# Optimization experiments

Hardware: AMD Instinct MI355X
Metric: run time of the kernel (lower is better)

Reference implementation:

```python
import jax, jax.numpy as jnp
import numpy as np

B, CI, CO, H, W, M1, M2 = 4, 64, 64, 256, 256, 16, 16


def setup_inputs() -> dict:
    key = jax.random.key(0)
    k0, k1, k2, k3, k4 = jax.random.split(key, 5)
    scale = 1.0 / (CI * CO)
    x = jax.random.normal(k0, (B, CI, H, W), dtype=jnp.float32)
    # torch.rand -> uniform [0,1), scaled; real/imag parts of complex weights
    w1r = scale * jax.random.uniform(k1, (CO, CI, M1, M2), dtype=jnp.float32)
    w1i = scale * jax.random.uniform(k2, (CO, CI, M1, M2), dtype=jnp.float32)
    w2r = scale * jax.random.uniform(k3, (CO, CI, M1, M2), dtype=jnp.float32)
    w2i = scale * jax.random.uniform(k4, (CO, CI, M1, M2), dtype=jnp.float32)
    return {"x": x, "w1r": w1r, "w1i": w1i, "w2r": w2r, "w2i": w2i}


def reference(x, w1r, w1i, w2r, w2i):
    b, ci, h, w = x.shape
    co, _, m1, m2 = w1r.shape
    wf = w // 2 + 1  # rfft width
    x_ft = jnp.fft.rfft2(x)                       # [b, ci, h, wf] complex
    xs = x_ft[:, :, :m1, :m2]                     # low-frequency slice
    w1 = w1r + 1j * w1i
    w2 = w2r + 1j * w2i
    o1 = jnp.einsum('bixy,ioxy->boxy', xs, w1)    # [b, co, m1, m2]
    o2 = jnp.einsum('bixy,ioxy->boxy', xs, w2)    # same slice, per original code
    out_ft = jnp.zeros((b, co, h, wf), dtype=x_ft.dtype)
    out_ft = out_ft.at[:, :, :m1, :m2].set(o1)
    out_ft = out_ft.at[:, :, h - m1:, :m2].set(o2)
    return jnp.fft.irfft2(out_ft, s=(h, w))
```

## Files before the change

### kernel.cpp

```cpp
#include <hip/hip_runtime.h>

#define NB 4
#define NCI 64
#define NCO 64
#define PLANE 65536

#define OF_XS_RE 0
#define OF_XS_IM (OF_XS_RE + PLANE)
#define OF_O1_RE (OF_XS_IM + PLANE)
#define OF_O1_IM (OF_O1_RE + PLANE)
#define OF_O2_RE (OF_O1_IM + PLANE)
#define OF_O2_IM (OF_O2_RE + PLANE)

#define XEOFF(w) ((w)*260)
#define XOOFF(w) (16*260 + 8 + (w)*260)

#define TPF 6.2831853071795864769f

__global__ __launch_bounds__(1024, 4) void k12_dft(const float* __restrict__ x,
                                                   float* __restrict__ ws) {
  __shared__ float bufA[8336], bufB[8336];
  __shared__ float cst[256], snt[256];
  __shared__ float2 s2[1024];
  const int t = threadIdx.x;
  const int img = blockIdx.x;

  if (t < 256) {
    float sv_, cv_;
    sincosf(TPF * (float)t * (1.0f/256.0f), &sv_, &cv_);
    cst[t] = cv_;  snt[t] = sv_;
  }

  const int sl = t & 3, row = t >> 2;
  const int wq = t & 3, p = (t >> 2) & 1;
  const int kg = (t >> 3) & 1, tr = t >> 4;
  int kyv[4];
#pragma unroll
  for (int j = 0; j < 4; ++j) kyv[j] = p + 8*kg + 2*j;

  const float* xb = x + (size_t)img * 65536;

  float4 lo0 = *(const float4*)(xb + row*256 + sl*4);
  float4 hi0 = *(const float4*)(xb + row*256 + 128 + sl*4);
  float4 lo1 = *(const float4*)(xb + row*256 + 16 + sl*4);
  float4 hi1 = *(const float4*)(xb + row*256 + 144 + sl*4);

  __syncthreads();

  float cd[4], sd[4];
#pragma unroll
  for (int j = 0; j < 4; ++j) { cd[j] = cst[kyv[j]]; sd[j] = snt[kyv[j]]; }

  float ar[4][4], ai[4][4];
#pragma unroll
  for (int j = 0; j < 4; ++j)
#pragma unroll
    for (int r = 0; r < 4; ++r) { ar[j][r] = 0.f; ai[j][r] = 0.f; }

  bufA[XEOFF(sl*4+0) + row] = lo0.x + hi0.x;
  bufA[XEOFF(sl*4+1) + row] = lo0.y + hi0.y;
  bufA[XEOFF(sl*4+2) + row] = lo0.z + hi0.z;
  bufA[XEOFF(sl*4+3) + row] = lo0.w + hi0.w;
  bufA[XOOFF(sl*4+0) + row] = lo0.x - hi0.x;
  bufA[XOOFF(sl*4+1) + row] = lo0.y - hi0.y;
  bufA[XOOFF(sl*4+2) + row] = lo0.z - hi0.z;
  bufA[XOOFF(sl*4+3) + row] = lo0.w - hi0.w;
  __syncthreads();

  const int pofs = p ? (16*260 + 8) : 0;

  for (int c = 0; c < 8; ++c) {
    float* cur = (c & 1) ? bufB : bufA;
    float* nxt = (c & 1) ? bufA : bufB;
    if (c < 6) {
      const int w0n = (c+2) * 16;
      if (c & 1) {
        lo1 = *(const float4*)(xb + row*256 + w0n + sl*4);
        hi1 = *(const float4*)(xb + row*256 + w0n + 128 + sl*4);
      } else {
        lo0 = *(const float4*)(xb + row*256 + w0n + sl*4);
        hi0 = *(const float4*)(xb + row*256 + w0n + 128 + sl*4);
      }
    }
    float cc[4], sv[4];
#pragma unroll
    for (int j = 0; j < 4; ++j) {
      const int m = (kyv[j] * (c*16 + wq*4)) & 255;
      cc[j] = cst[m];
      sv[j] = snt[m];
    }
    const float* rp = cur + pofs;
#pragma unroll
    for (int i = 0; i < 4; ++i) {
      const int wl = wq*4 + i;
      const float4 xs4 = *(const float4*)&rp[wl*260 + tr*4];
#pragma unroll
      for (int j = 0; j < 4; ++j) {
        ar[j][0] += xs4.x * cc[j];  ai[j][0] -= xs4.x * sv[j];
        ar[j][1] += xs4.y * cc[j];  ai[j][1] -= xs4.y * sv[j];
        ar[j][2] += xs4.z * cc[j];  ai[j][2] -= xs4.z * sv[j];
        ar[j][3] += xs4.w * cc[j];  ai[j][3] -= xs4.w * sv[j];
        const float nc = cc[j]*cd[j] - sv[j]*sd[j];
        const float ns = sv[j]*cd[j] + cc[j]*sd[j];
        cc[j] = nc; sv[j] = ns;
      }
    }
    if (c < 7) {
      if (c & 1) {
        nxt[XEOFF(sl*4+0) + row] = lo0.x + hi0.x;
        nxt[XEOFF(sl*4+1) + row] = lo0.y + hi0.y;
        nxt[XEOFF(sl*4+2) + row] = lo0.z + hi0.z;
        nxt[XEOFF(sl*4+3) + row] = lo0.w + hi0.w;
        nxt[XOOFF(sl*4+0) + row] = lo0.x - hi0.x;
        nxt[XOOFF(sl*4+1) + row] = lo0.y - hi0.y;
        nxt[XOOFF(sl*4+2) + row] = lo0.z - hi0.z;
        nxt[XOOFF(sl*4+3) + row] = lo0.w - hi0.w;
      } else {
        nxt[XEOFF(sl*4+0) + row] = lo1.x + hi1.x;
        nxt[XEOFF(sl*4+1) + row] = lo1.y + hi1.y;
        nxt[XEOFF(sl*4+2) + row] = lo1.z + hi1.z;
        nxt[XEOFF(sl*4+3) + row] = lo1.w + hi1.w;
        nxt[XOOFF(sl*4+0) + row] = lo1.x - hi1.x;
        nxt[XOOFF(sl*4+1) + row] = lo1.y - hi1.y;
        nxt[XOOFF(sl*4+2) + row] = lo1.z - hi1.z;
        nxt[XOOFF(sl*4+3) + row] = lo1.w - hi1.w;
      }
    }
    __syncthreads();
  }

#pragma unroll
  for (int j = 0; j < 4; ++j)
#pragma unroll
    for (int r = 0; r < 4; ++r) {
      ar[j][r] += __shfl_xor(ar[j][r], 1);
      ar[j][r] += __shfl_xor(ar[j][r], 2);
      ai[j][r] += __shfl_xor(ai[j][r], 1);
      ai[j][r] += __shfl_xor(ai[j][r], 2);
    }
  if (wq == 0) {
#pragma unroll
    for (int j = 0; j < 4; ++j) {
      const int ky = kyv[j];
      float4 sr; sr.x = ar[j][0]; sr.y = ar[j][1]; sr.z = ar[j][2]; sr.w = ar[j][3];
      float4 si; si.x = ai[j][0]; si.y = ai[j][1]; si.z = ai[j][2]; si.w = ai[j][3];
      *(float4*)&bufA[XEOFF(ky) + tr*4] = sr;
      *(float4*)&bufA[XOOFF(ky) + tr*4] = si;
    }
  }
  __syncthreads();

  const int ky2 = t & 15, kx = (t >> 4) & 15, hh = t >> 8;
  const float sg = (kx & 1) ? -1.f : 1.f;
  const float cdk = cst[kx], sdk = snt[kx];
  const int m0 = (kx * hh * 32) & 255;
  float cR = cst[m0], sR = snt[m0];
  float arr = 0.f, aii = 0.f;
  const int be = XEOFF(ky2) + hh*32;
  const int bo = XOOFF(ky2) + hh*32;
#pragma unroll 4
  for (int hq = 0; hq < 8; ++hq) {
    const float4 xrL = *(const float4*)&bufA[be + hq*4];
    const float4 xrH = *(const float4*)&bufA[be + 128 + hq*4];
    const float4 xiL = *(const float4*)&bufA[bo + hq*4];
    const float4 xiH = *(const float4*)&bufA[bo + 128 + hq*4];
    {
      const float xr = xrL.x + sg*xrH.x, xi = xiL.x + sg*xiH.x;
      arr += xr*cR + xi*sR;  aii += xi*cR - xr*sR;
      const float nc = cR*cdk - sR*sdk, ns = sR*cdk + cR*sdk; cR = nc; sR = ns;
    }
    {
      const float xr = xrL.y + sg*xrH.y, xi = xiL.y + sg*xiH.y;
      arr += xr*cR + xi*sR;  aii += xi*cR - xr*sR;
      const float nc = cR*cdk - sR*sdk, ns = sR*cdk + cR*sdk; cR = nc; sR = ns;
    }
    {
      const float xr = xrL.z + sg*xrH.z, xi = xiL.z + sg*xiH.z;
      arr += xr*cR + xi*sR;  aii += xi*cR - xr*sR;
      const float nc = cR*cdk - sR*sdk, ns = sR*cdk + cR*sdk; cR = nc; sR = ns;
    }
    {
      const float xr = xrL.w + sg*xrH.w, xi = xiL.w + sg*xiH.w;
      arr += xr*cR + xi*sR;  aii += xi*cR - xr*sR;
      const float nc = cR*cdk - sR*sdk, ns = sR*cdk + cR*sdk; cR = nc; sR = ns;
    }
  }
  s2[t].x = arr; s2[t].y = aii;
  __syncthreads();
  if (t < 256) {
    float xre = s2[t].x + s2[t+256].x + s2[t+512].x + s2[t+768].x;
    float xim = s2[t].y + s2[t+256].y + s2[t+512].y + s2[t+768].y;
    ws[OF_XS_RE + img*256 + t] = xre;
    ws[OF_XS_IM + img*256 + t] = xim;
  }
}

__global__ __launch_bounds__(256) void k3_mix(const float* __restrict__ w1r,
    const float* __restrict__ w1i, const float* __restrict__ w2r,
    const float* __restrict__ w2i, float* __restrict__ ws) {
  const int o  = blockIdx.x;
  const int mc = blockIdx.y;
  const int t  = threadIdx.x;
  const int b  = t >> 6;
  const int m  = (mc << 6) + (t & 63);
  const float* xsr = ws + OF_XS_RE;
  const float* xsi = ws + OF_XS_IM;
  float a1r=0.f, a1i=0.f, a2r=0.f, a2i=0.f;
#pragma unroll 4
  for (int i = 0; i < NCI; ++i) {
    const float xr = xsr[((b*NCI + i) << 8) + m];
    const float xi = xsi[((b*NCI + i) << 8) + m];
    const int wi = ((i*NCO + o) << 8) + m;
    const float p = w1r[wi], q = w1i[wi], u = w2r[wi], v = w2i[wi];
    a1r += xr*p - xi*q;
    a1i += xr*q + xi*p;
    a2r += xr*u - xi*v;
    a2i += xr*v + xi*u;
  }
  const int oi = ((b*NCO + o) << 8) + m;
  ws[OF_O1_RE + oi] = a1r;
  ws[OF_O1_IM + oi] = a1i;
  ws[OF_O2_RE + oi] = a2r;
  ws[OF_O2_IM + oi] = a2i;
}

__global__ __launch_bounds__(256) void k45_idft(const float* __restrict__ ws,
                                                float* __restrict__ out) {
  __shared__ __align__(16) float o1r[256], o1i[256], o2r[256], o2i[256];
  __shared__ float cst[256], snt[256];
  __shared__ __align__(16) float Sr[128][20], Si[128][20];
  const int t   = threadIdx.x;
  const int bo  = blockIdx.x >> 1;
  const int hcc = blockIdx.x & 1;

  o1r[t] = ws[OF_O1_RE + bo*256 + t];
  o1i[t] = ws[OF_O1_IM + bo*256 + t];
  o2r[t] = ws[OF_O2_RE + bo*256 + t];
  o2i[t] = ws[OF_O2_IM + bo*256 + t];
  {
    float sv_, cv_;
    sincosf(TPF * (float)t * (1.0f/256.0f), &sv_, &cv_);
    cst[t] = cv_;  snt[t] = sv_;
  }
  __syncthreads();

  {
    const int hl = t >> 2, kq = t & 3;
    const int h  = hcc*64 + hl;
    const float chh = cst[h], shh = snt[h];
    float c1 = 1.f, s1 = 0.f;
    const int m2i = (240 * h) & 255;
    float cB = cst[m2i], sB = snt[m2i];
    float4 srE = {0,0,0,0}, siE = {0,0,0,0};
    float4 srO = {0,0,0,0}, siO = {0,0,0,0};
#pragma unroll
    for (int j = 0; j < 16; ++j) {
      const float4 r1 = *(const float4*)&o1r[j*16 + kq*4];
      const float4 i1 = *(const float4*)&o1i[j*16 + kq*4];
      const float4 r2 = *(const float4*)&o2r[j*16 + kq*4];
      const float4 i2 = *(const float4*)&o2i[j*16 + kq*4];
      float4& sr = (j & 1) ? srO : srE;
      float4& si = (j & 1) ? siO : siE;
      sr.x += r1.x*c1 - i1.x*s1 + r2.x*cB - i2.x*sB;
      si.x += r1.x*s1 + i1.x*c1 + r2.x*sB + i2.x*cB;
      sr.y += r1.y*c1 - i1.y*s1 + r2.y*cB - i2.y*sB;
      si.y += r1.y*s1 + i1.y*c1 + r2.y*sB + i2.y*cB;
      sr.z += r1.z*c1 - i1.z*s1 + r2.z*cB - i2.z*sB;
      si.z += r1.z*s1 + i1.z*c1 + r2.z*sB + i2.z*cB;
      sr.w += r1.w*c1 - i1.w*s1 + r2.w*cB - i2.w*sB;
      si.w += r1.w*s1 + i1.w*c1 + r2.w*sB + i2.w*cB;
      const float n1c = c1*chh - s1*shh, n1s = s1*chh + c1*shh;
      const float n2c = cB*chh - sB*shh, n2s = sB*chh + cB*shh;
      c1 = n1c; s1 = n1s; cB = n2c; sB = n2s;
    }
    float4 sp, sm;
    sp.x = srE.x + srO.x; sp.y = srE.y + srO.y; sp.z = srE.z + srO.z; sp.w = srE.w + srO.w;
    sm.x = srE.x - srO.x; sm.y = srE.y - srO.y; sm.z = srE.z - srO.z; sm.w = srE.w - srO.w;
    *(float4*)&Sr[hl][kq*4]      = sp;
    *(float4*)&Sr[hl+64][kq*4]   = sm;
    sp.x = siE.x + siO.x; sp.y = siE.y + siO.y; sp.z = siE.z + siO.z; sp.w = siE.w + siO.w;
    sm.x = siE.x - siO.x; sm.y = siE.y - siO.y; sm.z = siE.z - siO.z; sm.w = siE.w - siO.w;
    *(float4*)&Si[hl][kq*4]      = sp;
    *(float4*)&Si[hl+64][kq*4]   = sm;
  }
  __syncthreads();

  const int wl = t & 31;
  float c[15], s[15], c2[15], s2[15];
#pragma unroll
  for (int k = 0; k < 15; ++k) {
    const int mi = ((k+1) * wl) & 255;
    c[k] = cst[mi];
    s[k] = snt[mi];
  }
  {
    const float R = 0.70710678118654752f;
#pragma unroll
    for (int k = 0; k < 15; ++k) {
      const int r8 = (k + 1) & 7;
      switch (r8) {
        case 0: c2[k] =  c[k];            s2[k] =  s[k];            break;
        case 1: c2[k] = (c[k]-s[k])*R;    s2[k] = (s[k]+c[k])*R;    break;
        case 2: c2[k] = -s[k];            s2[k] =  c[k];            break;
        case 3: c2[k] = -(c[k]+s[k])*R;   s2[k] = (c[k]-s[k])*R;    break;
        case 4: c2[k] = -c[k];            s2[k] = -s[k];            break;
        case 5: c2[k] = (s[k]-c[k])*R;    s2[k] = -(c[k]+s[k])*R;   break;
        case 6: c2[k] =  s[k];            s2[k] = -c[k];            break;
        default:c2[k] = (c[k]+s[k])*R;    s2[k] = (s[k]-c[k])*R;    break;
      }
    }
  }

  const int half = (t >> 5) & 1;
  const int wv = t >> 6;
  const float scale = 2.0f / 65536.0f;
  const size_t base256 = (size_t)bo*256 + hcc*64;
#pragma unroll 2
  for (int pr = 0; pr < 16; ++pr) {
    const int lr = wv*32 + pr*2 + half;
    const float4 a0 = *(const float4*)&Sr[lr][0];
    const float4 a1 = *(const float4*)&Sr[lr][4];
    const float4 a2 = *(const float4*)&Sr[lr][8];
    const float4 a3 = *(const float4*)&Sr[lr][12];
    const float4 b0 = *(const float4*)&Si[lr][0];
    const float4 b1 = *(const float4*)&Si[lr][4];
    const float4 b2 = *(const float4*)&Si[lr][8];
    const float4 b3 = *(const float4*)&Si[lr][12];
    const float re[16] = {a0.x,a0.y,a0.z,a0.w, a1.x,a1.y,a1.z,a1.w,
                          a2.x,a2.y,a2.z,a2.w, a3.x,a3.y,a3.z,a3.w};
    const float im[16] = {b0.x,b0.y,b0.z,b0.w, b1.x,b1.y,b1.z,b1.w,
                          b2.x,b2.y,b2.z,b2.w, b3.x,b3.y,b3.z,b3.w};
    const int grow = (lr & 63) + ((lr >> 6) << 7);
    const size_t ob = (base256 + grow) * 256;

#pragma unroll
    for (int g = 0; g < 2; ++g) {
      const float* cc = g ? c2 : c;
      const float* ss = g ? s2 : s;
      float PA = 0.5f * re[0];
      float PB = 0.f, PC = 0.f, PD = 0.f, QB = 0.f, QD = 0.f;
#pragma unroll
      for (int k = 0; k < 15; ++k) {
        const int ky = k + 1;
        const float R = re[ky], I = im[ky];
        const int cls = ky & 3;
        if (cls == 0)      PA += R*cc[k] - I*ss[k];
        else if (cls == 1) { PB += R*cc[k] - I*ss[k];  QB += R*ss[k] + I*cc[k]; }
        else if (cls == 2) PC += R*cc[k] - I*ss[k];
        else               { PD += R*cc[k] - I*ss[k];  QD += R*ss[k] + I*cc[k]; }
      }
      const float T1 = PA + PC, T2 = PB + PD;
      const float T3 = PA - PC, T4 = QB - QD;
      const int cb = wl + g*32;
      out[ob + cb]       = (T1 + T2) * scale;
      out[ob + cb + 64]  = (T3 - T4) * scale;
      out[ob + cb + 128] = (T1 - T2) * scale;
      out[ob + cb + 192] = (T3 + T4) * scale;
    }
  }
}

extern "C" void kernel_launch(void* const* d_in, const int* in_sizes, int n_in,
                              void* d_out, int out_size, void* d_ws, size_t ws_size,
                              hipStream_t stream) {
  const float* x   = (const float*)d_in[0];
  const float* w1r = (const float*)d_in[1];
  const float* w1i = (const float*)d_in[2];
  const float* w2r = (const float*)d_in[3];
  const float* w2i = (const float*)d_in[4];
  float* out = (float*)d_out;
  float* ws  = (float*)d_ws;

  hipLaunchKernelGGL(k12_dft,  dim3(256),   dim3(1024), 0, stream, x, ws);
  hipLaunchKernelGGL(k3_mix,   dim3(64, 4), dim3(256),  0, stream, w1r, w1i, w2r, w2i, ws);
  hipLaunchKernelGGL(k45_idft, dim3(512),   dim3(256),  0, stream, ws, out);
}
```

Before: 54.95 us.

## Fuse spectral channel mixing into the inverse DFT kernel

Removes the separate mixing kernel and computes the complex channel contraction for one (batch, out-channel) pair directly inside the inverse-DFT block, writing results to shared memory instead of the workspace. This drops one kernel launch and the global write/read of the intermediate spectra. In exchange, each mix result is computed twice (once per half-height block), and weights are re-read per batch block instead of being shared across batch within one block, increasing weight traffic.

Result: faster. 53.31 us (-3.0%).

```diff
diff --git a/kernel.cpp b/kernel.cpp
--- a/kernel.cpp
+++ b/kernel.cpp
@@ -7,10 +7,6 @@
 
 #define OF_XS_RE 0
 #define OF_XS_IM (OF_XS_RE + PLANE)
-#define OF_O1_RE (OF_XS_IM + PLANE)
-#define OF_O1_IM (OF_O1_RE + PLANE)
-#define OF_O2_RE (OF_O1_IM + PLANE)
-#define OF_O2_IM (OF_O2_RE + PLANE)
 
 #define XEOFF(w) ((w)*260)
 #define XOOFF(w) (16*260 + 8 + (w)*260)
@@ -195,37 +191,10 @@
   }
 }
 
-__global__ __launch_bounds__(256) void k3_mix(const float* __restrict__ w1r,
+__global__ __launch_bounds__(256) void k345_idft(const float* __restrict__ w1r,
     const float* __restrict__ w1i, const float* __restrict__ w2r,
-    const float* __restrict__ w2i, float* __restrict__ ws) {
-  const int o  = blockIdx.x;
-  const int mc = blockIdx.y;
-  const int t  = threadIdx.x;
-  const int b  = t >> 6;
-  const int m  = (mc << 6) + (t & 63);
-  const float* xsr = ws + OF_XS_RE;
-  const float* xsi = ws + OF_XS_IM;
-  float a1r=0.f, a1i=0.f, a2r=0.f, a2i=0.f;
-#pragma unroll 4
-  for (int i = 0; i < NCI; ++i) {
-    const float xr = xsr[((b*NCI + i) << 8) + m];
-    const float xi = xsi[((b*NCI + i) << 8) + m];
-    const int wi = ((i*NCO + o) << 8) + m;
-    const float p = w1r[wi], q = w1i[wi], u = w2r[wi], v = w2i[wi];
-    a1r += xr*p - xi*q;
-    a1i += xr*q + xi*p;
-    a2r += xr*u - xi*v;
-    a2i += xr*v + xi*u;
-  }
-  const int oi = ((b*NCO + o) << 8) + m;
-  ws[OF_O1_RE + oi] = a1r;
-  ws[OF_O1_IM + oi] = a1i;
-  ws[OF_O2_RE + oi] = a2r;
-  ws[OF_O2_IM + oi] = a2i;
-}
-
-__global__ __launch_bounds__(256) void k45_idft(const float* __restrict__ ws,
-                                                float* __restrict__ out) {
+    const float* __restrict__ w2i, const float* __restrict__ ws,
+    float* __restrict__ out) {
   __shared__ __align__(16) float o1r[256], o1i[256], o2r[256], o2i[256];
   __shared__ float cst[256], snt[256];
   __shared__ __align__(16) float Sr[128][20], Si[128][20];
@@ -233,14 +202,33 @@
   const int bo  = blockIdx.x >> 1;
   const int hcc = blockIdx.x & 1;
 
-  o1r[t] = ws[OF_O1_RE + bo*256 + t];
-  o1i[t] = ws[OF_O1_IM + bo*256 + t];
-  o2r[t] = ws[OF_O2_RE + bo*256 + t];
-  o2i[t] = ws[OF_O2_IM + bo*256 + t];
   {
     float sv_, cv_;
     sincosf(TPF * (float)t * (1.0f/256.0f), &sv_, &cv_);
     cst[t] = cv_;  snt[t] = sv_;
+  }
+
+  {
+    const int b = bo >> 6, o = bo & 63;
+    const float* xsr = ws + OF_XS_RE;
+    const float* xsi = ws + OF_XS_IM;
+    float a1r=0.f, a1i=0.f, a2r=0.f, a2i=0.f;
+#pragma unroll 4
+    for (int i = 0; i < NCI; ++i) {
+      const int xi_ = ((b*NCI + i) << 8) + t;
+      const float xr = xsr[xi_];
+      const float xi = xsi[xi_];
+      const int wi = ((i*NCO + o) << 8) + t;
+      const float pw = w1r[wi], q = w1i[wi], u = w2r[wi], v = w2i[wi];
+      a1r += xr*pw - xi*q;
+      a1i += xr*q + xi*pw;
+      a2r += xr*u - xi*v;
+      a2i += xr*v + xi*u;
+    }
+    o1r[t] = a1r;
+    o1i[t] = a1i;
+    o2r[t] = a2r;
+    o2i[t] = a2i;
   }
   __syncthreads();
 
@@ -371,7 +359,7 @@
   float* out = (float*)d_out;
   float* ws  = (float*)d_ws;
 
-  hipLaunchKernelGGL(k12_dft,  dim3(256),   dim3(1024), 0, stream, x, ws);
-  hipLaunchKernelGGL(k3_mix,   dim3(64, 4), dim3(256),  0, stream, w1r, w1i, w2r, w2i, ws);
-  hipLaunchKernelGGL(k45_idft, dim3(512),   dim3(256),  0, stream, ws, out);
+  hipLaunchKernelGGL(k12_dft,   dim3(256), dim3(1024), 0, stream, x, ws);
+  hipLaunchKernelGGL(k345_idft, dim3(512), dim3(256),  0, stream,
+                     w1r, w1i, w2r, w2i, ws, out);
 }
```
